# Kernel optimization log

Hardware: AMD Instinct MI355X
Metric: run time of the kernel (lower is better)

## Reference

```python
import jax, jax.numpy as jnp
import numpy as np

B, N, I, O, H = 4, 2048, 256, 128, 8
THRESHOLD = 0.5
NEG = -1e10

def setup_inputs() -> dict:
    key = jax.random.key(0)
    ks = jax.random.split(key, 9)
    s = 0.05
    return {
        'h': jax.random.normal(ks[0], (B, N, I), dtype=jnp.float32),
        'adj': jax.random.uniform(ks[1], (B, N, N), dtype=jnp.float32),
        'conv_w': jax.random.normal(ks[2], (H, O, I), dtype=jnp.float32) * s,
        'conv_b': jax.random.normal(ks[3], (H, O), dtype=jnp.float32) * s,
        'a': jax.random.normal(ks[4], (H, 2 * O), dtype=jnp.float32) * s,
        'Wh1_bias': jax.random.normal(ks[5], (H, N, 1), dtype=jnp.float32) * s,
        'Wh2_bias': jax.random.normal(ks[6], (H, N, 1), dtype=jnp.float32) * s,
        'a_bias': jax.random.normal(ks[7], (H, N, N), dtype=jnp.float32) * s,
        'attention_bias': jax.random.normal(ks[8], (H, N, O), dtype=jnp.float32) * s,
    }

def reference(h, adj, conv_w, conv_b, a, Wh1_bias, Wh2_bias, a_bias, attention_bias):
    # Per-head 1x1 conv == per-head linear: (B,N,I) x (H,O,I) -> (B,H,N,O)
    Wh = jnp.einsum('bni,hoi->bhno', h, conv_w) + conv_b[None, :, None, :]
    a1 = a[:, :O]   # (H,O)
    a2 = a[:, O:]   # (H,O)
    Wh1 = jnp.einsum('bhno,ho->bhn', Wh, a1)[..., None] + Wh1_bias            # (B,H,N,1)
    # torch 'bhno,hol->bhln' transposes to (B,H,1,N); adding (H,N,1) bias broadcasts to (B,H,N,N)
    Wh2 = jnp.einsum('bhno,ho->bhn', Wh, a2)[:, :, None, :] + Wh2_bias[None]  # (B,H,N,N)
    e = jax.nn.leaky_relu(Wh1 + Wh2, negative_slope=0.2) + a_bias             # (B,H,N,N)
    scores = jnp.where(adj[:, None] >= THRESHOLD, e, NEG)
    att = jax.nn.softmax(scores, axis=3)                                      # (B,H,N,N)
    # torch.einsum('bhnn,bhno->bhno') takes the DIAGONAL of attention (repeated label)
    diag = jnp.diagonal(att, axis1=2, axis2=3)                                # (B,H,N)
    h_prime = jax.nn.elu(diag[..., None] * Wh + attention_bias)               # (B,H,N,O)
    return h_prime.transpose(0, 2, 1, 3).reshape(B, N, H * O)
```

## Files before the change

### kernel.cpp

```cpp
#include <hip/hip_runtime.h>

constexpr int B_ = 4, N_ = 2048, I_ = 256, O_ = 128, H_ = 8;
constexpr int KC = 32;

__global__ __launch_bounds__(256) void gemm_mask(
    const float* __restrict__ hin, const float* __restrict__ cw,
    const float* __restrict__ cb, const float* __restrict__ a,
    const float* __restrict__ wb1, const float* __restrict__ wb2,
    const float* __restrict__ adj,
    float* __restrict__ Wh, float* __restrict__ u, float* __restrict__ v,
    unsigned char* __restrict__ nb)
{
  __shared__ float hsT[KC][64];
  __shared__ float wT[KC][128];
  const int tid = threadIdx.x;

  if (blockIdx.x >= 1024) {
    const int row  = (blockIdx.x - 1024) * 4 + (tid >> 6);
    const int lane = tid & 63;
    const float* arow = &adj[(size_t)row * N_];
    unsigned char* nrow = &nb[(size_t)row * 512];
    #pragma unroll
    for (int it = 0; it < 8; ++it) {
      int g = it * 64 + lane;
      float4 a4 = *(const float4*)&arow[g * 4];
      unsigned int nib = (unsigned int)(a4.x >= 0.5f)
                       | ((unsigned int)(a4.y >= 0.5f) << 1)
                       | ((unsigned int)(a4.z >= 0.5f) << 2)
                       | ((unsigned int)(a4.w >= 0.5f) << 3);
      nrow[g] = (unsigned char)nib;
    }
    return;
  }

  const int bid = blockIdx.x;
  const int n0  = (bid & 31) * 64;
  const int by  = bid >> 5;
  const int b   = by >> 3;
  const int hh  = by & 7;
  const int tn  = tid >> 4;
  const int to  = tid & 15;

  float acc[4][8];
  #pragma unroll
  for (int j = 0; j < 4; ++j)
    #pragma unroll
    for (int c = 0; c < 8; ++c) acc[j][c] = 0.f;

  for (int i0 = 0; i0 < I_; i0 += KC) {
    __syncthreads();
    #pragma unroll
    for (int kk = 0; kk < 2; ++kk) {
      int f4 = tid + kk * 256;
      int n  = f4 >> 3;
      int i4 = (f4 & 7) * 4;
      float4 hv = *(const float4*)&hin[((size_t)(b * N_ + n0 + n)) * I_ + i0 + i4];
      hsT[i4 + 0][n] = hv.x; hsT[i4 + 1][n] = hv.y;
      hsT[i4 + 2][n] = hv.z; hsT[i4 + 3][n] = hv.w;
    }
    #pragma unroll
    for (int kk = 0; kk < 4; ++kk) {
      int f4 = tid + kk * 256;
      int o  = f4 >> 3;
      int i4 = (f4 & 7) * 4;
      float4 wv = *(const float4*)&cw[((size_t)(hh * O_ + o)) * I_ + i0 + i4];
      wT[i4 + 0][o] = wv.x; wT[i4 + 1][o] = wv.y;
      wT[i4 + 2][o] = wv.z; wT[i4 + 3][o] = wv.w;
    }
    __syncthreads();
    #pragma unroll
    for (int k = 0; k < KC; ++k) {
      float4 av  = *(const float4*)&hsT[k][tn * 4];
      float4 b0  = *(const float4*)&wT[k][to * 4];
      float4 b1v = *(const float4*)&wT[k][to * 4 + 64];
      float aj;
      #define FMA_ROW(J, COMP)                                            \
        aj = COMP;                                                        \
        acc[J][0] = fmaf(aj, b0.x,  acc[J][0]);                           \
        acc[J][1] = fmaf(aj, b0.y,  acc[J][1]);                           \
        acc[J][2] = fmaf(aj, b0.z,  acc[J][2]);                           \
        acc[J][3] = fmaf(aj, b0.w,  acc[J][3]);                           \
        acc[J][4] = fmaf(aj, b1v.x, acc[J][4]);                           \
        acc[J][5] = fmaf(aj, b1v.y, acc[J][5]);                           \
        acc[J][6] = fmaf(aj, b1v.z, acc[J][6]);                           \
        acc[J][7] = fmaf(aj, b1v.w, acc[J][7]);
      FMA_ROW(0, av.x) FMA_ROW(1, av.y) FMA_ROW(2, av.z) FMA_ROW(3, av.w)
      #undef FMA_ROW
    }
  }

  {
    float4 cb0 = *(const float4*)&cb[hh * O_ + to * 4];
    float4 cb1 = *(const float4*)&cb[hh * O_ + to * 4 + 64];
    #pragma unroll
    for (int j = 0; j < 4; ++j) {
      acc[j][0] += cb0.x; acc[j][1] += cb0.y; acc[j][2] += cb0.z; acc[j][3] += cb0.w;
      acc[j][4] += cb1.x; acc[j][5] += cb1.y; acc[j][6] += cb1.z; acc[j][7] += cb1.w;
    }
  }

  const float* ah = &a[hh * 2 * O_];
  float4 a1l = *(const float4*)&ah[to * 4];
  float4 a1h = *(const float4*)&ah[64 + to * 4];
  float4 a2l = *(const float4*)&ah[128 + to * 4];
  float4 a2h = *(const float4*)&ah[192 + to * 4];

  #pragma unroll
  for (int j = 0; j < 4; ++j) {
    int n = n0 + tn * 4 + j;
    size_t base = (((size_t)(b * N_ + n)) * H_ + hh) * O_;
    *(float4*)&Wh[base + to * 4]      = make_float4(acc[j][0], acc[j][1], acc[j][2], acc[j][3]);
    *(float4*)&Wh[base + to * 4 + 64] = make_float4(acc[j][4], acc[j][5], acc[j][6], acc[j][7]);

    float pu = acc[j][0]*a1l.x + acc[j][1]*a1l.y + acc[j][2]*a1l.z + acc[j][3]*a1l.w
             + acc[j][4]*a1h.x + acc[j][5]*a1h.y + acc[j][6]*a1h.z + acc[j][7]*a1h.w;
    float pv = acc[j][0]*a2l.x + acc[j][1]*a2l.y + acc[j][2]*a2l.z + acc[j][3]*a2l.w
             + acc[j][4]*a2h.x + acc[j][5]*a2h.y + acc[j][6]*a2h.z + acc[j][7]*a2h.w;
    #pragma unroll
    for (int off = 8; off; off >>= 1) {
      pu += __shfl_xor(pu, off);
      pv += __shfl_xor(pv, off);
    }
    if (to == 0) {
      int idx = (b * H_ + hh) * N_ + n;
      u[idx] = pu + wb1[hh * N_ + n] + wb2[hh * N_ + n];
      v[idx] = pv;
    }
  }
}

__global__ __launch_bounds__(256) void attn_fused(
    const unsigned char* __restrict__ nb, const float* __restrict__ abias,
    const float* __restrict__ u, const float* __restrict__ v,
    const float* __restrict__ Wh, const float* __restrict__ attb,
    float* __restrict__ out)
{
  const int r    = blockIdx.x;
  const int hh   = blockIdx.y;
  const int lane = threadIdx.x & 63;
  const int b    = threadIdx.x >> 6;
  const int bh   = b * H_ + hh;

  const float uval = u[bh * N_ + r];
  const float* vrow  = &v[(size_t)bh * N_];
  const float* abrow = &abias[((size_t)(hh * N_ + r)) * N_];
  const unsigned char* nrow = &nb[(size_t)(b * N_ + r) * 512];

  float ss = 0.f;
  #pragma unroll
  for (int kk = 0; kk < 8; ++kk) {
    int c4 = kk * 256 + lane * 4;
    float4 v4 = *(const float4*)&vrow[c4];
    float4 a4 = *(const float4*)&abrow[c4];
    unsigned int nib = nrow[kk * 64 + lane];
    float pre, lr, e;
    #define COL(J, VC, AC)                                                \
      pre = uval + VC;                                                    \
      lr  = fmaxf(pre, 0.2f * pre);                                      \
      e   = __expf(lr + AC);                                              \
      ss += (nib & (1u << J)) ? e : 0.f;
    COL(0, v4.x, a4.x) COL(1, v4.y, a4.y)
    COL(2, v4.z, a4.z) COL(3, v4.w, a4.w)
    #undef COL
  }
  #pragma unroll
  for (int off = 32; off; off >>= 1) ss += __shfl_xor(ss, off);

  float prd = uval + vrow[r];
  float lrd = fmaxf(prd, 0.2f * prd);
  unsigned int nibd = nrow[r >> 2];
  float diag = (nibd & (1u << (r & 3))) ? __expf(lrd + abrow[r]) / ss : 0.f;

  size_t obase = (((size_t)(b * N_ + r)) * H_ + hh) * O_;
  const float* atr = &attb[((size_t)(hh * N_ + r)) * O_];
  #pragma unroll
  for (int t = 0; t < 2; ++t) {
    int oo = lane + 64 * t;
    float x = diag * Wh[obase + oo] + atr[oo];
    out[obase + oo] = x > 0.f ? x : __expf(x) - 1.f;
  }
}

extern "C" void kernel_launch(void* const* d_in, const int* in_sizes, int n_in,
                              void* d_out, int out_size, void* d_ws, size_t ws_size,
                              hipStream_t stream) {
  const float* hin   = (const float*)d_in[0];
  const float* adj   = (const float*)d_in[1];
  const float* cw    = (const float*)d_in[2];
  const float* cb    = (const float*)d_in[3];
  const float* a     = (const float*)d_in[4];
  const float* wb1   = (const float*)d_in[5];
  const float* wb2   = (const float*)d_in[6];
  const float* abias = (const float*)d_in[7];
  const float* attb  = (const float*)d_in[8];
  float* out = (float*)d_out;

  float* u = (float*)d_ws;
  float* v = u + (size_t)B_ * H_ * N_;
  unsigned char* nb = (unsigned char*)(v + (size_t)B_ * H_ * N_);
  float* whws = (float*)(nb + (size_t)B_ * N_ * 512);

  size_t needBytes = ((size_t)B_ * H_ * N_ * 2) * 4 + (size_t)B_ * N_ * 512
                   + (size_t)B_ * N_ * H_ * O_ * 4;
  float* Wh = (ws_size >= needBytes) ? whws : out;

  gemm_mask<<<dim3(1024 + B_ * N_ / 4), 256, 0, stream>>>(
      hin, cw, cb, a, wb1, wb2, adj, Wh, u, v, nb);
  attn_fused<<<dim3(N_, H_), 256, 0, stream>>>(nb, abias, u, v, Wh, attb, out);
}
```

Measured before the change: 348.2 us.

## Enlarge GEMM tile, repack mask bytes, use exp2 and hoist loads in attention

The GEMM tile grows from 64 to 128 rows per block, with padded shared-memory strides, halving the block count and doubling register accumulators. The adjacency mask is packed into a 64-bit word per lane so each lane does one 8-byte store, and the attention kernel reads it back with one uint2 load. u and v are prescaled by log2(e) so the attention kernel can use hardware exp2. All row loads are issued up front and four independent partial sums are kept to improve memory-level parallelism. Higher register use in the GEMM may lower occupancy.

```diff
diff --git a/kernel.cpp b/kernel.cpp
--- a/kernel.cpp
+++ b/kernel.cpp
@@ -1,7 +1,11 @@
 #include <hip/hip_runtime.h>
 
 constexpr int B_ = 4, N_ = 2048, I_ = 256, O_ = 128, H_ = 8;
-constexpr int KC = 32;
+constexpr float LOG2E = 1.4426950408889634f;
+constexpr int LDP = 132;
+constexpr int GEMM_BLOCKS = 512;
+
+#define EXP2(x) __builtin_amdgcn_exp2f(x)
 
 __global__ __launch_bounds__(256) void gemm_mask(
     const float* __restrict__ hin, const float* __restrict__ cw,
@@ -11,94 +15,88 @@
     float* __restrict__ Wh, float* __restrict__ u, float* __restrict__ v,
     unsigned char* __restrict__ nb)
 {
-  __shared__ float hsT[KC][64];
-  __shared__ float wT[KC][128];
+  __shared__ float hsT[32 * LDP];
+  __shared__ float wT[32 * LDP];
   const int tid = threadIdx.x;
 
-  if (blockIdx.x >= 1024) {
-    const int row  = (blockIdx.x - 1024) * 4 + (tid >> 6);
-    const int lane = tid & 63;
+  if (blockIdx.x >= GEMM_BLOCKS) {
+    const int row = (blockIdx.x - GEMM_BLOCKS) * 4 + (tid >> 6);
+    const int ml  = tid & 63;
     const float* arow = &adj[(size_t)row * N_];
-    unsigned char* nrow = &nb[(size_t)row * 512];
+    unsigned long long acc64 = 0ull;
     #pragma unroll
     for (int it = 0; it < 8; ++it) {
-      int g = it * 64 + lane;
+      int g = it * 64 + ml;
       float4 a4 = *(const float4*)&arow[g * 4];
-      unsigned int nib = (unsigned int)(a4.x >= 0.5f)
-                       | ((unsigned int)(a4.y >= 0.5f) << 1)
-                       | ((unsigned int)(a4.z >= 0.5f) << 2)
-                       | ((unsigned int)(a4.w >= 0.5f) << 3);
-      nrow[g] = (unsigned char)nib;
-    }
+      unsigned long long nib =
+          (unsigned long long)(a4.x >= 0.5f)
+        | ((unsigned long long)(a4.y >= 0.5f) << 1)
+        | ((unsigned long long)(a4.z >= 0.5f) << 2)
+        | ((unsigned long long)(a4.w >= 0.5f) << 3);
+      acc64 |= nib << (8 * it);
+    }
+    *(unsigned long long*)&nb[(size_t)row * 512 + ml * 8] = acc64;
     return;
   }
 
   const int bid = blockIdx.x;
-  const int n0  = (bid & 31) * 64;
-  const int by  = bid >> 5;
+  const int n0  = (bid & 15) * 128;
+  const int by  = bid >> 4;
   const int b   = by >> 3;
   const int hh  = by & 7;
   const int tn  = tid >> 4;
   const int to  = tid & 15;
 
-  float acc[4][8];
-  #pragma unroll
-  for (int j = 0; j < 4; ++j)
-    #pragma unroll
-    for (int c = 0; c < 8; ++c) acc[j][c] = 0.f;
-
-  for (int i0 = 0; i0 < I_; i0 += KC) {
+  float acc[2][4][8];
+  #pragma unroll
+  for (int g = 0; g < 2; ++g)
+    #pragma unroll
+    for (int j = 0; j < 4; ++j)
+      #pragma unroll
+      for (int c = 0; c < 8; ++c) acc[g][j][c] = 0.f;
+
+  for (int i0 = 0; i0 < I_; i0 += 32) {
     __syncthreads();
     #pragma unroll
-    for (int kk = 0; kk < 2; ++kk) {
+    for (int kk = 0; kk < 4; ++kk) {
       int f4 = tid + kk * 256;
       int n  = f4 >> 3;
       int i4 = (f4 & 7) * 4;
       float4 hv = *(const float4*)&hin[((size_t)(b * N_ + n0 + n)) * I_ + i0 + i4];
-      hsT[i4 + 0][n] = hv.x; hsT[i4 + 1][n] = hv.y;
-      hsT[i4 + 2][n] = hv.z; hsT[i4 + 3][n] = hv.w;
-    }
-    #pragma unroll
-    for (int kk = 0; kk < 4; ++kk) {
-      int f4 = tid + kk * 256;
-      int o  = f4 >> 3;
-      int i4 = (f4 & 7) * 4;
-      float4 wv = *(const float4*)&cw[((size_t)(hh * O_ + o)) * I_ + i0 + i4];
-      wT[i4 + 0][o] = wv.x; wT[i4 + 1][o] = wv.y;
-      wT[i4 + 2][o] = wv.z; wT[i4 + 3][o] = wv.w;
+      hsT[(i4 + 0) * LDP + n] = hv.x; hsT[(i4 + 1) * LDP + n] = hv.y;
+      hsT[(i4 + 2) * LDP + n] = hv.z; hsT[(i4 + 3) * LDP + n] = hv.w;
+      float4 wv = *(const float4*)&cw[((size_t)(hh * O_ + n)) * I_ + i0 + i4];
+      wT[(i4 + 0) * LDP + n] = wv.x; wT[(i4 + 1) * LDP + n] = wv.y;
+      wT[(i4 + 2) * LDP + n] = wv.z; wT[(i4 + 3) * LDP + n] = wv.w;
     }
     __syncthreads();
-    #pragma unroll
-    for (int k = 0; k < KC; ++k) {
-      float4 av  = *(const float4*)&hsT[k][tn * 4];
-      float4 b0  = *(const float4*)&wT[k][to * 4];
-      float4 b1v = *(const float4*)&wT[k][to * 4 + 64];
+    #pragma unroll 8
+    for (int k = 0; k < 32; ++k) {
+      const float* hr = &hsT[k * LDP];
+      const float* wr = &wT[k * LDP];
+      float4 av0 = *(const float4*)&hr[tn * 4];
+      float4 av1 = *(const float4*)&hr[64 + tn * 4];
+      float4 bv0 = *(const float4*)&wr[to * 4];
+      float4 bv1 = *(const float4*)&wr[64 + to * 4];
       float aj;
-      #define FMA_ROW(J, COMP)                                            \
+      #define FMA_ROW(G, J, COMP)                                         \
         aj = COMP;                                                        \
-        acc[J][0] = fmaf(aj, b0.x,  acc[J][0]);                           \
-        acc[J][1] = fmaf(aj, b0.y,  acc[J][1]);                           \
-        acc[J][2] = fmaf(aj, b0.z,  acc[J][2]);                           \
-        acc[J][3] = fmaf(aj, b0.w,  acc[J][3]);                           \
-        acc[J][4] = fmaf(aj, b1v.x, acc[J][4]);                           \
-        acc[J][5] = fmaf(aj, b1v.y, acc[J][5]);                           \
-        acc[J][6] = fmaf(aj, b1v.z, acc[J][6]);                           \
-        acc[J][7] = fmaf(aj, b1v.w, acc[J][7]);
-      FMA_ROW(0, av.x) FMA_ROW(1, av.y) FMA_ROW(2, av.z) FMA_ROW(3, av.w)
+        acc[G][J][0] = fmaf(aj, bv0.x, acc[G][J][0]);                     \
+        acc[G][J][1] = fmaf(aj, bv0.y, acc[G][J][1]);                     \
+        acc[G][J][2] = fmaf(aj, bv0.z, acc[G][J][2]);                     \
+        acc[G][J][3] = fmaf(aj, bv0.w, acc[G][J][3]);                     \
+        acc[G][J][4] = fmaf(aj, bv1.x, acc[G][J][4]);                     \
+        acc[G][J][5] = fmaf(aj, bv1.y, acc[G][J][5]);                     \
+        acc[G][J][6] = fmaf(aj, bv1.z, acc[G][J][6]);                     \
+        acc[G][J][7] = fmaf(aj, bv1.w, acc[G][J][7]);
+      FMA_ROW(0, 0, av0.x) FMA_ROW(0, 1, av0.y) FMA_ROW(0, 2, av0.z) FMA_ROW(0, 3, av0.w)
+      FMA_ROW(1, 0, av1.x) FMA_ROW(1, 1, av1.y) FMA_ROW(1, 2, av1.z) FMA_ROW(1, 3, av1.w)
       #undef FMA_ROW
     }
   }
 
-  {
-    float4 cb0 = *(const float4*)&cb[hh * O_ + to * 4];
-    float4 cb1 = *(const float4*)&cb[hh * O_ + to * 4 + 64];
-    #pragma unroll
-    for (int j = 0; j < 4; ++j) {
-      acc[j][0] += cb0.x; acc[j][1] += cb0.y; acc[j][2] += cb0.z; acc[j][3] += cb0.w;
-      acc[j][4] += cb1.x; acc[j][5] += cb1.y; acc[j][6] += cb1.z; acc[j][7] += cb1.w;
-    }
-  }
-
+  float4 cb0 = *(const float4*)&cb[hh * O_ + to * 4];
+  float4 cb1 = *(const float4*)&cb[hh * O_ + to * 4 + 64];
   const float* ah = &a[hh * 2 * O_];
   float4 a1l = *(const float4*)&ah[to * 4];
   float4 a1h = *(const float4*)&ah[64 + to * 4];
@@ -106,25 +104,31 @@
   float4 a2h = *(const float4*)&ah[192 + to * 4];
 
   #pragma unroll
-  for (int j = 0; j < 4; ++j) {
-    int n = n0 + tn * 4 + j;
-    size_t base = (((size_t)(b * N_ + n)) * H_ + hh) * O_;
-    *(float4*)&Wh[base + to * 4]      = make_float4(acc[j][0], acc[j][1], acc[j][2], acc[j][3]);
-    *(float4*)&Wh[base + to * 4 + 64] = make_float4(acc[j][4], acc[j][5], acc[j][6], acc[j][7]);
-
-    float pu = acc[j][0]*a1l.x + acc[j][1]*a1l.y + acc[j][2]*a1l.z + acc[j][3]*a1l.w
-             + acc[j][4]*a1h.x + acc[j][5]*a1h.y + acc[j][6]*a1h.z + acc[j][7]*a1h.w;
-    float pv = acc[j][0]*a2l.x + acc[j][1]*a2l.y + acc[j][2]*a2l.z + acc[j][3]*a2l.w
-             + acc[j][4]*a2h.x + acc[j][5]*a2h.y + acc[j][6]*a2h.z + acc[j][7]*a2h.w;
-    #pragma unroll
-    for (int off = 8; off; off >>= 1) {
-      pu += __shfl_xor(pu, off);
-      pv += __shfl_xor(pv, off);
-    }
-    if (to == 0) {
-      int idx = (b * H_ + hh) * N_ + n;
-      u[idx] = pu + wb1[hh * N_ + n] + wb2[hh * N_ + n];
-      v[idx] = pv;
+  for (int g = 0; g < 2; ++g) {
+    #pragma unroll
+    for (int j = 0; j < 4; ++j) {
+      float* A = acc[g][j];
+      A[0] += cb0.x; A[1] += cb0.y; A[2] += cb0.z; A[3] += cb0.w;
+      A[4] += cb1.x; A[5] += cb1.y; A[6] += cb1.z; A[7] += cb1.w;
+      int n = n0 + g * 64 + tn * 4 + j;
+      size_t base = (((size_t)(b * N_ + n)) * H_ + hh) * O_;
+      *(float4*)&Wh[base + to * 4]      = make_float4(A[0], A[1], A[2], A[3]);
+      *(float4*)&Wh[base + to * 4 + 64] = make_float4(A[4], A[5], A[6], A[7]);
+
+      float pu = A[0]*a1l.x + A[1]*a1l.y + A[2]*a1l.z + A[3]*a1l.w
+               + A[4]*a1h.x + A[5]*a1h.y + A[6]*a1h.z + A[7]*a1h.w;
+      float pv = A[0]*a2l.x + A[1]*a2l.y + A[2]*a2l.z + A[3]*a2l.w
+               + A[4]*a2h.x + A[5]*a2h.y + A[6]*a2h.z + A[7]*a2h.w;
+      #pragma unroll
+      for (int off = 8; off; off >>= 1) {
+        pu += __shfl_xor(pu, off);
+        pv += __shfl_xor(pv, off);
+      }
+      if (to == 0) {
+        int idx = (b * H_ + hh) * N_ + n;
+        u[idx] = (pu + wb1[hh * N_ + n] + wb2[hh * N_ + n]) * LOG2E;
+        v[idx] = pv * LOG2E;
+      }
     }
   }
 }
@@ -141,44 +145,56 @@
   const int b    = threadIdx.x >> 6;
   const int bh   = b * H_ + hh;
 
-  const float uval = u[bh * N_ + r];
   const float* vrow  = &v[(size_t)bh * N_];
   const float* abrow = &abias[((size_t)(hh * N_ + r)) * N_];
   const unsigned char* nrow = &nb[(size_t)(b * N_ + r) * 512];
 
-  float ss = 0.f;
+  uint2 mk = *(const uint2*)&nrow[lane * 8];
+  float4 vv[8], aa[8];
   #pragma unroll
   for (int kk = 0; kk < 8; ++kk) {
     int c4 = kk * 256 + lane * 4;
-    float4 v4 = *(const float4*)&vrow[c4];
-    float4 a4 = *(const float4*)&abrow[c4];
-    unsigned int nib = nrow[kk * 64 + lane];
+    vv[kk] = *(const float4*)&vrow[c4];
+    aa[kk] = *(const float4*)&abrow[c4];
+  }
+  const size_t obase = (((size_t)(b * N_ + r)) * H_ + hh) * O_;
+  const float* atr = &attb[((size_t)(hh * N_ + r)) * O_];
+  float wh0 = Wh[obase + lane], wh1 = Wh[obase + lane + 64];
+  float at0 = atr[lane],        at1 = atr[lane + 64];
+  float uval = u[bh * N_ + r];
+  float vdiag = vrow[r];
+
+  float ss0 = 0.f, ss1 = 0.f, ss2 = 0.f, ss3 = 0.f;
+  #pragma unroll
+  for (int kk = 0; kk < 8; ++kk) {
+    unsigned int nib =
+        (kk < 4 ? (mk.x >> (kk * 8)) : (mk.y >> ((kk - 4) * 8))) & 0xffu;
+    float4 v4 = vv[kk], a4 = aa[kk];
     float pre, lr, e;
-    #define COL(J, VC, AC)                                                \
+    #define COL(J, VC, AC, SS)                                            \
       pre = uval + VC;                                                    \
-      lr  = fmaxf(pre, 0.2f * pre);                                      \
-      e   = __expf(lr + AC);                                              \
-      ss += (nib & (1u << J)) ? e : 0.f;
-    COL(0, v4.x, a4.x) COL(1, v4.y, a4.y)
-    COL(2, v4.z, a4.z) COL(3, v4.w, a4.w)
+      lr  = fmaxf(pre, 0.2f * pre);                                       \
+      e   = EXP2(fmaf(AC, LOG2E, lr));                                    \
+      SS += (nib & (1u << J)) ? e : 0.f;
+    COL(0, v4.x, a4.x, ss0) COL(1, v4.y, a4.y, ss1)
+    COL(2, v4.z, a4.z, ss2) COL(3, v4.w, a4.w, ss3)
     #undef COL
   }
+  float ss = (ss0 + ss1) + (ss2 + ss3);
   #pragma unroll
   for (int off = 32; off; off >>= 1) ss += __shfl_xor(ss, off);
 
-  float prd = uval + vrow[r];
+  int gd = r >> 2;
+  unsigned int nibd = nrow[(gd & 63) * 8 + (gd >> 6)];
+  float prd = uval + vdiag;
   float lrd = fmaxf(prd, 0.2f * prd);
-  unsigned int nibd = nrow[r >> 2];
-  float diag = (nibd & (1u << (r & 3))) ? __expf(lrd + abrow[r]) / ss : 0.f;
-
-  size_t obase = (((size_t)(b * N_ + r)) * H_ + hh) * O_;
-  const float* atr = &attb[((size_t)(hh * N_ + r)) * O_];
-  #pragma unroll
-  for (int t = 0; t < 2; ++t) {
-    int oo = lane + 64 * t;
-    float x = diag * Wh[obase + oo] + atr[oo];
-    out[obase + oo] = x > 0.f ? x : __expf(x) - 1.f;
-  }
+  float numd = EXP2(fmaf(abrow[r], LOG2E, lrd));
+  float diag = ((nibd >> (r & 3)) & 1u) ? numd / ss : 0.f;
+
+  float x0 = fmaf(diag, wh0, at0);
+  float x1 = fmaf(diag, wh1, at1);
+  out[obase + lane]      = x0 > 0.f ? x0 : __expf(x0) - 1.f;
+  out[obase + lane + 64] = x1 > 0.f ? x1 : __expf(x1) - 1.f;
 }
 
 extern "C" void kernel_launch(void* const* d_in, const int* in_sizes, int n_in,
@@ -204,7 +220,7 @@
                    + (size_t)B_ * N_ * H_ * O_ * 4;
   float* Wh = (ws_size >= needBytes) ? whws : out;
 
-  gemm_mask<<<dim3(1024 + B_ * N_ / 4), 256, 0, stream>>>(
+  gemm_mask<<<dim3(GEMM_BLOCKS + B_ * N_ / 4), 256, 0, stream>>>(
       hin, cw, cb, a, wb1, wb2, adj, Wh, u, v, nb);
   attn_fused<<<dim3(N_, H_), 256, 0, stream>>>(nb, abias, u, v, Wh, attb, out);
 }
```

After: 352.6 us. About the same (+1.3%).
